# Performance work log

Hardware: AMD Instinct MI355X
Metric: run time of the kernel (lower is better)

The kernel has to match this reference:

```python
import jax, jax.numpy as jnp
import numpy as np

N_NODES = 20000   # atoms
N_EDGES = 320000  # bonds = line-graph nodes
N_ANGLES = 640000 # line-graph edges
N_GRAPHS = 256
NF = 92           # node_features
EF = 40           # edge_features (= RBF/ABF bins)
FC = 256
LAYERS = 3


def _bn(x, g, b):
    # BatchNorm1d in training mode: batch stats, biased variance, eps=1e-5
    mu = jnp.mean(x, axis=0)
    var = jnp.var(x, axis=0)
    return g * (x - mu) * jax.lax.rsqrt(var + 1e-5) + b


def _rbf(x, vmin, vmax, bins):
    centers = jnp.linspace(vmin, vmax, bins)
    gamma = 1.0 / (centers[1] - centers[0])  # 1/lengthscale (ALIGNN RBFExpansion)
    return jnp.exp(-gamma * (x[:, None] - centers) ** 2)


def _conv(src, dst, n_nodes, nf, ef, Ws, bs, Wd, bd, We, be, gm, bm, gn, bn2):
    # CGCNN conv: gather(u_add_v) + edge linear + BN + gated act + scatter-sum + BN + softplus residual
    h_src = nf @ Ws + bs                       # [N, 2F]
    h_dst = nf @ Wd + bd                       # [N, 2F]
    m = h_src[src] + h_dst[dst] + ef @ We + be # [E, 2F]
    m = _bn(m, gm, bm)
    h_f, h_s = jnp.split(m, 2, axis=1)
    m = jax.nn.sigmoid(h_f) * jax.nn.softplus(h_s)          # [E, F]
    h = jax.ops.segment_sum(m, dst, num_segments=n_nodes)   # scatter-sum to dst nodes
    h = _bn(h, gn, bn2)
    return jax.nn.softplus(nf + h)


def setup_inputs() -> dict:
    key = jax.random.key(0)
    ks = iter(jax.random.split(key, 64))
    rn = lambda *s: jax.random.normal(next(ks), s, dtype=jnp.float32)
    d = {}
    d['atom_features'] = rn(N_NODES, NF)
    d['r'] = rn(N_EDGES, 3) * 2.0  # bond vectors; norms land within RBF range [0, 8]
    d['angle_h'] = ((jax.random.uniform(next(ks), (N_ANGLES,), dtype=jnp.float32) - 0.5) * np.pi)
    d['g_src'] = jax.random.randint(next(ks), (N_EDGES,), 0, N_NODES, dtype=jnp.int32)
    d['g_dst'] = jax.random.randint(next(ks), (N_EDGES,), 0, N_NODES, dtype=jnp.int32)
    d['lg_src'] = jax.random.randint(next(ks), (N_ANGLES,), 0, N_EDGES, dtype=jnp.int32)
    d['lg_dst'] = jax.random.randint(next(ks), (N_ANGLES,), 0, N_EDGES, dtype=jnp.int32)
    d['node_gid'] = jnp.sort(jax.random.randint(next(ks), (N_NODES,), 0, N_GRAPHS, dtype=jnp.int32))
    d['emb_W'] = rn(NF, NF) * 0.1
    d['emb_b'] = jnp.zeros((NF,), jnp.float32)
    # conv layers on atom graph: node dim NF, edge dim EF, out 2*NF
    d['c1_Wsrc'] = rn(LAYERS, NF, 2 * NF) * 0.1
    d['c1_bsrc'] = jnp.zeros((LAYERS, 2 * NF), jnp.float32)
    d['c1_Wdst'] = rn(LAYERS, NF, 2 * NF) * 0.1
    d['c1_bdst'] = jnp.zeros((LAYERS, 2 * NF), jnp.float32)
    d['c1_Wedge'] = rn(LAYERS, EF, 2 * NF) * 0.1
    d['c1_bedge'] = jnp.zeros((LAYERS, 2 * NF), jnp.float32)
    d['c1_bnm_g'] = jnp.ones((LAYERS, 2 * NF), jnp.float32)
    d['c1_bnm_b'] = jnp.zeros((LAYERS, 2 * NF), jnp.float32)
    d['c1_bn_g'] = jnp.ones((LAYERS, NF), jnp.float32)
    d['c1_bn_b'] = jnp.zeros((LAYERS, NF), jnp.float32)
    # conv layers on line graph: node dim EF, edge dim EF, out 2*EF
    d['c2_Wsrc'] = rn(LAYERS, EF, 2 * EF) * 0.1
    d['c2_bsrc'] = jnp.zeros((LAYERS, 2 * EF), jnp.float32)
    d['c2_Wdst'] = rn(LAYERS, EF, 2 * EF) * 0.1
    d['c2_bdst'] = jnp.zeros((LAYERS, 2 * EF), jnp.float32)
    d['c2_Wedge'] = rn(LAYERS, EF, 2 * EF) * 0.1
    d['c2_bedge'] = jnp.zeros((LAYERS, 2 * EF), jnp.float32)
    d['c2_bnm_g'] = jnp.ones((LAYERS, 2 * EF), jnp.float32)
    d['c2_bnm_b'] = jnp.zeros((LAYERS, 2 * EF), jnp.float32)
    d['c2_bn_g'] = jnp.ones((LAYERS, EF), jnp.float32)
    d['c2_bn_b'] = jnp.zeros((LAYERS, EF), jnp.float32)
    d['fc_W'] = rn(NF, FC) * 0.1
    d['fc_b'] = jnp.zeros((FC,), jnp.float32)
    d['out_W'] = rn(FC, 1) * 0.1
    d['out_b'] = jnp.zeros((1,), jnp.float32)
    return d


def reference(atom_features, r, angle_h, g_src, g_dst, lg_src, lg_dst, node_gid,
              emb_W, emb_b,
              c1_Wsrc, c1_bsrc, c1_Wdst, c1_bdst, c1_Wedge, c1_bedge,
              c1_bnm_g, c1_bnm_b, c1_bn_g, c1_bn_b,
              c2_Wsrc, c2_bsrc, c2_Wdst, c2_bdst, c2_Wedge, c2_bedge,
              c2_bnm_g, c2_bnm_b, c2_bn_g, c2_bn_b,
              fc_W, fc_b, out_W, out_b):
    angle_features = _rbf(angle_h, -np.pi / 2, np.pi / 2, EF)      # [E2, EF]
    bondlength = jnp.linalg.norm(r, axis=1)                        # [E]
    edge_features = _rbf(bondlength, 0.0, 8.0, EF)                 # [E, EF]
    node_features = atom_features @ emb_W + emb_b                  # [N, NF]
    for i in range(LAYERS):
        node_features = _conv(g_src, g_dst, N_NODES, node_features, edge_features,
                              c1_Wsrc[i], c1_bsrc[i], c1_Wdst[i], c1_bdst[i],
                              c1_Wedge[i], c1_bedge[i], c1_bnm_g[i], c1_bnm_b[i],
                              c1_bn_g[i], c1_bn_b[i])
        edge_features = _conv(lg_src, lg_dst, N_EDGES, edge_features, angle_features,
                              c2_Wsrc[i], c2_bsrc[i], c2_Wdst[i], c2_bdst[i],
                              c2_Wedge[i], c2_bedge[i], c2_bnm_g[i], c2_bnm_b[i],
                              c2_bn_g[i], c2_bn_b[i])
    # AvgPooling readout over nodes per graph
    sums = jax.ops.segment_sum(node_features, node_gid, num_segments=N_GRAPHS)
    cnts = jax.ops.segment_sum(jnp.ones((N_NODES,), node_features.dtype), node_gid, num_segments=N_GRAPHS)
    feats = sums / jnp.maximum(cnts, 1.0)[:, None]                 # [G, NF]
    feats = jax.nn.softplus(feats)
    feats = jax.nn.softplus(feats @ fc_W + fc_b)                   # fc = Linear + Softplus, then extra softplus
    feats = jax.nn.softplus(feats)
    out = feats @ out_W + out_b                                    # [G, 1], link = identity
    return jnp.squeeze(out, axis=-1)                               # [G]
```

## Files before the change

### kernel.cpp

```cpp
#include <hip/hip_runtime.h>
#include <math.h>

#define N_NODES   20000
#define N_EDGESC  320000
#define N_ANGLESC 640000
#define N_GRAPHSC 256
#define NFDIM     92
#define EFDIM     40
#define FCDIM     256

typedef unsigned short u16;
typedef unsigned int u32;
typedef __attribute__((ext_vector_type(8))) short bf16x8;
typedef __attribute__((ext_vector_type(4))) float f32x4;

__device__ __forceinline__ u16 f2bf(float x) {
  union { float f; unsigned u; } v; v.f = x;
  unsigned r = v.u + 0x7fff + ((v.u >> 16) & 1);
  return (u16)(r >> 16);
}
__device__ __forceinline__ float bf2f(u16 h) {
  union { unsigned u; float f; } v; v.u = ((unsigned)h) << 16; return v.f;
}
__device__ __forceinline__ u32 pk2(float a, float b) {
  return (u32)f2bf(a) | ((u32)f2bf(b) << 16);
}
__device__ __forceinline__ float fsp(float x) {
  float e = __expf(-fabsf(x));
  return fmaxf(x, 0.f) + __logf(1.f + e);
}
__device__ __forceinline__ float fsig(float x) {
  float e = __expf(-x);
  return __builtin_amdgcn_rcpf(1.f + e);
}

__global__ void k_hist(const int* __restrict__ dst, int E, int* __restrict__ hist) {
  int e = blockIdx.x * blockDim.x + threadIdx.x;
  if (e < E) atomicAdd(&hist[dst[e]], 1);
}

__global__ void k_scan_pass1(const int* __restrict__ hist, int n, int* __restrict__ bsum) {
  __shared__ int buf[256];
  int i = blockIdx.x * 256 + threadIdx.x;
  buf[threadIdx.x] = (i < n) ? hist[i] : 0;
  __syncthreads();
  for (int o = 128; o > 0; o >>= 1) {
    if (threadIdx.x < o) buf[threadIdx.x] += buf[threadIdx.x + o];
    __syncthreads();
  }
  if (threadIdx.x == 0) bsum[blockIdx.x] = buf[0];
}

__global__ void k_scan_partials(int* __restrict__ bsum, int B) {
  __shared__ int buf[256];
  __shared__ int carry;
  if (threadIdx.x == 0) carry = 0;
  __syncthreads();
  for (int base = 0; base < B; base += 256) {
    int i = base + threadIdx.x;
    int v = (i < B) ? bsum[i] : 0;
    buf[threadIdx.x] = v;
    __syncthreads();
    for (int o = 1; o < 256; o <<= 1) {
      int t = (threadIdx.x >= o) ? buf[threadIdx.x - o] : 0;
      __syncthreads();
      buf[threadIdx.x] += t;
      __syncthreads();
    }
    if (i < B) bsum[i] = buf[threadIdx.x] - v + carry;
    int tile_total = buf[255];
    __syncthreads();
    if (threadIdx.x == 0) carry += tile_total;
    __syncthreads();
  }
}

__global__ void k_scan_pass3(const int* __restrict__ hist, int n, int total,
                             const int* __restrict__ bsum,
                             int* __restrict__ offsets, int* __restrict__ cursor) {
  __shared__ int buf[256];
  int i = blockIdx.x * 256 + threadIdx.x;
  int v = (i < n) ? hist[i] : 0;
  buf[threadIdx.x] = v;
  __syncthreads();
  for (int o = 1; o < 256; o <<= 1) {
    int t = (threadIdx.x >= o) ? buf[threadIdx.x - o] : 0;
    __syncthreads();
    buf[threadIdx.x] += t;
    __syncthreads();
  }
  int excl = buf[threadIdx.x] - v + bsum[blockIdx.x];
  if (i < n) {
    offsets[i] = excl;
    cursor[i] = excl;
    if (i == n - 1) offsets[n] = total;
  }
}

__global__ void k_fill(const int* __restrict__ dst, int E,
                       int* __restrict__ cursor, int* __restrict__ perm) {
  int e = blockIdx.x * blockDim.x + threadIdx.x;
  if (e >= E) return;
  int pos = atomicAdd(&cursor[dst[e]], 1);
  perm[pos] = e;
}

__global__ void k_sortbins(const int* __restrict__ offsets, int* __restrict__ perm, int nb) {
  int n = blockIdx.x * blockDim.x + threadIdx.x;
  if (n >= nb) return;
  int lo = offsets[n], hi = offsets[n + 1];
  for (int i = lo + 1; i < hi; i++) {
    int key = perm[i];
    int j = i - 1;
    while (j >= lo && perm[j] > key) { perm[j + 1] = perm[j]; j--; }
    perm[j + 1] = key;
  }
}

__global__ void k_invperm(const int* __restrict__ perm, int E, int* __restrict__ iperm) {
  int p = blockIdx.x * blockDim.x + threadIdx.x;
  if (p < E) iperm[perm[p]] = p;
}

__global__ void k_rbf_edge(const float* __restrict__ r, u16* __restrict__ ef) {
  int e = blockIdx.x * blockDim.x + threadIdx.x;
  if (e >= N_EDGESC) return;
  float x = r[e * 3 + 0], y = r[e * 3 + 1], z = r[e * 3 + 2];
  float bl = sqrtf(x * x + y * y + z * z);
  const float step = 8.f / 39.f;
  const float g = 39.f / 8.f;
  u32* o = (u32*)(ef + (long long)e * EFDIM);
#pragma unroll
  for (int i = 0; i < 20; i++) {
    float d0 = bl - (2 * i + 0) * step;
    float d1 = bl - (2 * i + 1) * step;
    o[i] = pk2(__expf(-g * d0 * d0), __expf(-g * d1 * d1));
  }
}

__global__ void k_gemm_bias(const float* __restrict__ A, const float* __restrict__ W,
                            const float* __restrict__ b, float* __restrict__ C,
                            int M, int N, int K) {
  int idx = blockIdx.x * blockDim.x + threadIdx.x;
  int total = M * N;
  if (idx >= total) return;
  int row = idx / N, col = idx - row * N;
  const float* a = A + (long long)row * K;
  float acc = b[col];
#pragma unroll 4
  for (int k = 0; k < K; k++) acc += a[k] * W[k * N + col];
  C[idx] = acc;
}

__global__ __launch_bounds__(256) void k_nf_gemm_b(
    const float* __restrict__ A, const float* __restrict__ W,
    const float* __restrict__ bias, u16* __restrict__ OUT) {
  __shared__ float As[64][93];
  __shared__ float Wls[92][64];
  __shared__ float bls[64];
  int t = threadIdx.x;
  int row0 = blockIdx.x * 64;
  int ct = blockIdx.y * 64;
  int cvalid = 184 - ct; if (cvalid > 64) cvalid = 64;
  for (int idx = t; idx < 64 * 92; idx += 256) {
    int rr = idx / 92, k = idx - rr * 92;
    int rg = row0 + rr;
    As[rr][k] = (rg < N_NODES) ? A[(long long)rg * 92 + k] : 0.f;
  }
  for (int idx = t; idx < 92 * 64; idx += 256) {
    int k = idx >> 6, c = idx & 63;
    Wls[k][c] = (c < cvalid) ? W[k * 184 + ct + c] : 0.f;
  }
  if (t < 64) bls[t] = (t < cvalid) ? bias[ct + t] : 0.f;
  __syncthreads();
  int rg = t >> 4, cg = t & 15;
  int r0 = rg * 4, c0 = cg * 4;
  float acc[4][4] = {};
#pragma unroll 2
  for (int k = 0; k < 92; k++) {
    float a0 = As[r0][k], a1 = As[r0 + 1][k], a2 = As[r0 + 2][k], a3 = As[r0 + 3][k];
    float4 w = *(float4*)&Wls[k][c0];
    acc[0][0] += a0 * w.x; acc[0][1] += a0 * w.y; acc[0][2] += a0 * w.z; acc[0][3] += a0 * w.w;
    acc[1][0] += a1 * w.x; acc[1][1] += a1 * w.y; acc[1][2] += a1 * w.z; acc[1][3] += a1 * w.w;
    acc[2][0] += a2 * w.x; acc[2][1] += a2 * w.y; acc[2][2] += a2 * w.z; acc[2][3] += a2 * w.w;
    acc[3][0] += a3 * w.x; acc[3][1] += a3 * w.y; acc[3][2] += a3 * w.z; acc[3][3] += a3 * w.w;
  }
  if (c0 < cvalid) {
    float b0 = bls[c0], b1 = bls[c0 + 1], b2 = bls[c0 + 2], b3 = bls[c0 + 3];
#pragma unroll
    for (int i = 0; i < 4; i++) {
      int rg2 = row0 + r0 + i;
      if (rg2 < N_NODES) {
        uint2 pkd;
        pkd.x = pk2(acc[i][0] + b0, acc[i][1] + b1);
        pkd.y = pk2(acc[i][2] + b2, acc[i][3] + b3);
        *(uint2*)(OUT + (long long)rg2 * 184 + ct + c0) = pkd;
      }
    }
  }
}

__global__ void k_mkwt1(const float* __restrict__ We, const float* __restrict__ be,
                        u16* __restrict__ WT1) {
  int idx = blockIdx.x * blockDim.x + threadIdx.x;
  if (idx >= 192 * 64) return;
  int c = idx >> 6, k = idx & 63;
  float v = 0.f;
  if (c < 184) {
    if (k < 40) v = We[k * 184 + c];
    else if (k == 40) v = be[c];
  }
  int b = 2 * k;
  int off = c * 128 + (((b >> 4) ^ (c & 7)) << 4) + (b & 15);
  WT1[off >> 1] = f2bf(v);
}

__global__ void k_mkwt2(const float* __restrict__ Ws, const float* __restrict__ bs,
                        const float* __restrict__ Wd, const float* __restrict__ bd,
                        const float* __restrict__ We, const float* __restrict__ be,
                        u16* __restrict__ WT2) {
  int idx = blockIdx.x * blockDim.x + threadIdx.x;
  if (idx >= 80 * 128) return;
  int c = idx >> 7, k = idx & 127;
  float v = 0.f;
  if (k < 40) v = Ws[k * 80 + c];
  else if (k < 80) v = Wd[(k - 40) * 80 + c];
  else if (k < 120) v = We[(k - 80) * 80 + c];
  else if (k == 120) v = bs[c] + bd[c] + be[c];
  int b = 2 * k;
  int off = c * 256 + (((b >> 4) ^ (c & 7)) << 4) + (b & 15);
  WT2[off >> 1] = f2bf(v);
}

__global__ __launch_bounds__(256) void k_conv1_mfma(
    const u16* __restrict__ EF, const int* __restrict__ src, const int* __restrict__ dst,
    const u16* __restrict__ HSb, const u16* __restrict__ HDb,
    const u16* __restrict__ WT1, const int* __restrict__ IPERM,
    u16* __restrict__ M, float* __restrict__ PART) {
  __shared__ __align__(16) char sA[64 * 128];
  __shared__ __align__(16) char sB[192 * 128];
  __shared__ float ssum[2][192];
  __shared__ int srcs[64], dsts[64], ipm[64];
  int t = threadIdx.x;
  int e0 = blockIdx.x * 64;
  for (int i = t; i < 2 * 192; i += 256) ((float*)ssum)[i] = 0.f;
  if (t < 64) {
    srcs[t] = src[e0 + t];
    dsts[t] = dst[e0 + t];
    ipm[t] = IPERM[e0 + t];
    uint4 z5 = {0x00003F80u, 0u, 0u, 0u};
    uint4 z = {0u, 0u, 0u, 0u};
    *(uint4*)(sA + t * 128 + ((5 ^ (t & 7)) << 4)) = z5;
    *(uint4*)(sA + t * 128 + ((6 ^ (t & 7)) << 4)) = z;
    *(uint4*)(sA + t * 128 + ((7 ^ (t & 7)) << 4)) = z;
  }
  {
    const uint4* efg = (const uint4*)EF;
    for (int i = t; i < 320; i += 256) {
      int r = i / 5, ch = i % 5;
      uint4 v = efg[(long long)(e0 + r) * 5 + ch];
      *(uint4*)(sA + r * 128 + ((ch ^ (r & 7)) << 4)) = v;
    }
  }
  {
    const uint4* wg = (const uint4*)WT1;
    uint4* bb = (uint4*)sB;
    for (int i = t; i < 1536; i += 256) bb[i] = wg[i];
  }
  __syncthreads();

  int lane = t & 63, w = t >> 6;
  int lr = lane & 15, lg = lane >> 4;
  int arow = w * 16 + lr;
  f32x4 zero = {0.f, 0.f, 0.f, 0.f};
  f32x4 acc[12];
#pragma unroll
  for (int n = 0; n < 12; n++) acc[n] = zero;
#pragma unroll
  for (int kt = 0; kt < 2; kt++) {
    bf16x8 a = *(const bf16x8*)(sA + arow * 128 + (((kt * 4 + lg) ^ (arow & 7)) << 4));
#pragma unroll
    for (int n = 0; n < 12; n++) {
      int brow = n * 16 + lr;
      bf16x8 b = *(const bf16x8*)(sB + brow * 128 + (((kt * 4 + lg) ^ (brow & 7)) << 4));
      acc[n] = __builtin_amdgcn_mfma_f32_16x16x32_bf16(a, b, acc[n], 0, 0, 0);
    }
  }
  __syncthreads();
  u16* stage = (u16*)sB;
  int base_r = w * 16 + lg * 4;
#pragma unroll
  for (int n = 0; n < 12; n++) {
    int col = n * 16 + lr;
    bool valid = col < 184;
    int pos = (col < 92) ? (2 * col) : (2 * (col - 92) + 1);
    float s = 0.f, q = 0.f;
#pragma unroll
    for (int j = 0; j < 4; j++) {
      int rr = base_r + j;
      float v = acc[n][j];
      if (valid) {
        v += bf2f(HSb[(long long)srcs[rr] * 184 + col]) + bf2f(HDb[(long long)dsts[rr] * 184 + col]);
        stage[rr * 192 + pos] = f2bf(v);
        s += v; q += v * v;
      }
    }
    s += __shfl_xor(s, 16, 64); s += __shfl_xor(s, 32, 64);
    q += __shfl_xor(q, 16, 64); q += __shfl_xor(q, 32, 64);
    if (valid && lg == 0) {
      atomicAdd(&ssum[0][col], s);
      atomicAdd(&ssum[1][col], q);
    }
  }
  __syncthreads();
  for (int i = t; i < 64 * 23; i += 256) {
    int rr = i / 23, ch = i - rr * 23;
    *(uint4*)(M + (long long)ipm[rr] * 184 + ch * 8) = *(const uint4*)(stage + rr * 192 + ch * 8);
  }
  float* P = PART + (long long)blockIdx.x * 368;
  for (int i = t; i < 184; i += 256) { P[i] = ssum[0][i]; P[184 + i] = ssum[1][i]; }
}

__global__ __launch_bounds__(256) void k_conv2_mfma(
    const u16* __restrict__ EF, const float* __restrict__ angle_h,
    const int* __restrict__ lsrc, const int* __restrict__ ldst,
    const u16* __restrict__ WT2, const int* __restrict__ IPERM,
    u16* __restrict__ M, float* __restrict__ PART) {
  __shared__ __align__(16) char sA[64 * 256];
  __shared__ __align__(16) char sB[80 * 256];
  __shared__ float ssum[2][80];
  __shared__ int srcl[64], dstl[64], ipm[64];
  __shared__ float hh[64];
  int t = threadIdx.x;
  int a0 = blockIdx.x * 64;
  if (t < 64) {
    srcl[t] = lsrc[a0 + t]; dstl[t] = ldst[a0 + t];
    hh[t] = angle_h[a0 + t]; ipm[t] = IPERM[a0 + t];
  }
  for (int i = t; i < 160; i += 256) ((float*)ssum)[i] = 0.f;
  __syncthreads();
  int lane = t & 63, w = t >> 6;
  if (w == 0) {
    int r = lane;
    const uint4* g = (const uint4*)EF + (long long)srcl[r] * 5;
#pragma unroll
    for (int ch = 0; ch < 5; ch++)
      *(uint4*)(sA + r * 256 + ((ch ^ (r & 7)) << 4)) = g[ch];
  } else if (w == 1) {
    int r = lane;
    const uint4* g = (const uint4*)EF + (long long)dstl[r] * 5;
#pragma unroll
    for (int ch = 0; ch < 5; ch++)
      *(uint4*)(sA + r * 256 + (((ch + 5) ^ (r & 7)) << 4)) = g[ch];
  } else {
    int r = lane;
    const float PI = 3.14159265358979323846f;
    const float step = PI / 39.f;
    const float gam = 39.f / PI;
    float h = hh[r];
    int k0 = (w == 2) ? 0 : 20;
#pragma unroll
    for (int p = 0; p < 10; p++) {
      int k = k0 + 2 * p;
      float d0 = h - (-PI * 0.5f + k * step);
      float d1 = h - (-PI * 0.5f + (k + 1) * step);
      u32 val = pk2(__expf(-gam * d0 * d0), __expf(-gam * d1 * d1));
      int b = 160 + 2 * k;
      *(u32*)(sA + r * 256 + (((b >> 4) ^ (r & 7)) << 4) + (b & 15)) = val;
    }
    if (w == 3) {
      uint4 z15 = {0x00003F80u, 0u, 0u, 0u};
      *(uint4*)(sA + r * 256 + ((15 ^ (r & 7)) << 4)) = z15;
    }
  }
  {
    const uint4* wg = (const uint4*)WT2;
    uint4* bb = (uint4*)sB;
    for (int i = t; i < 1280; i += 256) bb[i] = wg[i];
  }
  __syncthreads();

  int lr = lane & 15, lg = lane >> 4;
  int arow = w * 16 + lr;
  f32x4 zero = {0.f, 0.f, 0.f, 0.f};
  f32x4 acc[5];
#pragma unroll
  for (int n = 0; n < 5; n++) acc[n] = zero;
#pragma unroll
  for (int kt = 0; kt < 4; kt++) {
    bf16x8 a = *(const bf16x8*)(sA + arow * 256 + (((kt * 4 + lg) ^ (arow & 7)) << 4));
#pragma unroll
    for (int n = 0; n < 5; n++) {
      int brow = n * 16 + lr;
      bf16x8 b = *(const bf16x8*)(sB + brow * 256 + (((kt * 4 + lg) ^ (brow & 7)) << 4));
      acc[n] = __builtin_amdgcn_mfma_f32_16x16x32_bf16(a, b, acc[n], 0, 0, 0);
    }
  }
  __syncthreads();
  u16* stage = (u16*)sB;
  int base_r = w * 16 + lg * 4;
#pragma unroll
  for (int n = 0; n < 5; n++) {
    int col = n * 16 + lr;
    int pos = (col < 40) ? (2 * col) : (2 * (col - 40) + 1);
    float s = 0.f, q = 0.f;
#pragma unroll
    for (int j = 0; j < 4; j++) {
      float v = acc[n][j];
      stage[(base_r + j) * 80 + pos] = f2bf(v);
      s += v; q += v * v;
    }
    s += __shfl_xor(s, 16, 64); s += __shfl_xor(s, 32, 64);
    q += __shfl_xor(q, 16, 64); q += __shfl_xor(q, 32, 64);
    if (lg == 0) {
      atomicAdd(&ssum[0][col], s);
      atomicAdd(&ssum[1][col], q);
    }
  }
  __syncthreads();
  for (int i = t; i < 64 * 10; i += 256) {
    int rr = i / 10, ch = i - rr * 10;
    *(uint4*)(M + (long long)ipm[rr] * 80 + ch * 8) = *(const uint4*)(stage + rr * 80 + ch * 8);
  }
  float* P = PART + (long long)blockIdx.x * 160;
  for (int i = t; i < 80; i += 256) { P[i] = ssum[0][i]; P[80 + i] = ssum[1][i]; }
}

__global__ __launch_bounds__(256) void k_reduce_part(
    const float* __restrict__ part, int nblk, int C2, float* __restrict__ stat) {
  int chunks = gridDim.x;
  int per = (nblk + chunks - 1) / chunks;
  int lo = blockIdx.x * per;
  int hi = lo + per; if (hi > nblk) hi = nblk;
  if (lo >= hi) return;
  for (int c = threadIdx.x; c < C2; c += blockDim.x) {
    float s = 0.f;
    for (int b = lo; b < hi; b++) s += part[(long long)b * C2 + c];
    atomicAdd(&stat[c], s);
  }
}

__global__ void k_finalize(float* __restrict__ stat, const float* __restrict__ g,
                           const float* __restrict__ b, float* __restrict__ scsh,
                           int C, float invR) {
  int c = threadIdx.x + blockIdx.x * blockDim.x;
  if (c >= C) return;
  float mu = stat[c] * invR;
  float var = stat[C + c] * invR - mu * mu;
  float is = rsqrtf(var + 1e-5f);
  float sc = g[c] * is;
  scsh[c] = sc;
  scsh[C + c] = b[c] - mu * sc;
  stat[c] = 0.f;
  stat[C + c] = 0.f;
}

__global__ __launch_bounds__(512) void k_gather1(
    const u16* __restrict__ m, const int* __restrict__ offsets,
    const float* __restrict__ scsh, float* __restrict__ hagg, float* __restrict__ part) {
  __shared__ float sacc[4][92];
  int t = threadIdx.x;
  int ln = t >> 7, c = t & 127;
  int n = blockIdx.x * 4 + ln;
  if (c < 92) {
    float sc_f = scsh[c],       sh_f = scsh[184 + c];
    float sc_s = scsh[92 + c],  sh_s = scsh[276 + c];
    int lo = offsets[n], hi = offsets[n + 1];
    float acc = 0.f;
    for (int p = lo; p < hi; ++p) {
      u32 pr = *(const u32*)(m + (long long)p * 184 + 2 * c);
      float mf = bf2f((u16)(pr & 0xffffu)) * sc_f + sh_f;
      float ms = bf2f((u16)(pr >> 16)) * sc_s + sh_s;
      acc += fsig(mf) * fsp(ms);
    }
    hagg[(long long)n * 92 + c] = acc;
    sacc[ln][c] = acc;
  }
  __syncthreads();
  if (t < 184) {
    int cc = (t < 92) ? t : t - 92;
    bool sq = t >= 92;
    float s = 0.f;
#pragma unroll
    for (int b = 0; b < 4; b++) { float v = sacc[b][cc]; s += sq ? v * v : v; }
    part[(long long)blockIdx.x * 184 + t] = s;
  }
}

__global__ __launch_bounds__(320) void k_gather2(
    const u16* __restrict__ m, const int* __restrict__ offsets,
    const float* __restrict__ scsh, u16* __restrict__ hagg, float* __restrict__ part) {
  __shared__ float sacc[8][40];
  int t = threadIdx.x;
  int le = t / 40, c = t - le * 40;
  int e = blockIdx.x * 8 + le;
  float sc_f = scsh[c],      sh_f = scsh[80 + c];
  float sc_s = scsh[40 + c], sh_s = scsh[120 + c];
  int lo = offsets[e], hi = offsets[e + 1];
  float acc = 0.f;
  for (int p = lo; p < hi; ++p) {
    u32 pr = *(const u32*)(m + (long long)p * 80 + 2 * c);
    float mf = bf2f((u16)(pr & 0xffffu)) * sc_f + sh_f;
    float ms = bf2f((u16)(pr >> 16)) * sc_s + sh_s;
    acc += fsig(mf) * fsp(ms);
  }
  hagg[(long long)e * 40 + c] = f2bf(acc);
  sacc[le][c] = acc;
  __syncthreads();
  if (t < 80) {
    int cc = (t < 40) ? t : t - 40;
    bool sq = t >= 40;
    float s = 0.f;
#pragma unroll
    for (int b = 0; b < 8; b++) { float v = sacc[b][cc]; s += sq ? v * v : v; }
    part[(long long)blockIdx.x * 80 + t] = s;
  }
}

__global__ void k_bn_residual(const float* __restrict__ xin, const float* __restrict__ hagg,
                              const float* __restrict__ scsh, float* __restrict__ out,
                              int total, int C) {
  int idx = blockIdx.x * blockDim.x + threadIdx.x;
  if (idx >= total) return;
  int c = idx % C;
  out[idx] = fsp(xin[idx] + hagg[idx] * scsh[c] + scsh[C + c]);
}

__global__ void k_bn_residual_bb(u16* __restrict__ ef, const u16* __restrict__ hagg,
                                 const float* __restrict__ scsh, int total, int C) {
  int idx = blockIdx.x * blockDim.x + threadIdx.x;
  if (idx >= total) return;
  int c = idx % C;
  float v = fsp(bf2f(ef[idx]) + bf2f(hagg[idx]) * scsh[c] + scsh[C + c]);
  ef[idx] = f2bf(v);
}

__global__ __launch_bounds__(256) void k_head(
    const float* __restrict__ nf, const int* __restrict__ gid,
    const float* __restrict__ fcW, const float* __restrict__ fcb,
    const float* __restrict__ outW, const float* __restrict__ outb,
    float* __restrict__ out) {
  __shared__ float feats[NFDIM];
  __shared__ float warpsum[4];
  int g = blockIdx.x, t = threadIdx.x;
  int lo = 0, hi = N_NODES;
  while (lo < hi) { int mid = (lo + hi) >> 1; if (gid[mid] < g) lo = mid + 1; else hi = mid; }
  int lo2 = lo, hi2 = N_NODES;
  while (lo2 < hi2) { int mid = (lo2 + hi2) >> 1; if (gid[mid] < g + 1) lo2 = mid + 1; else hi2 = mid; }
  if (t < NFDIM) {
    float s = 0.f;
    for (int n = lo; n < lo2; ++n) s += nf[(long long)n * NFDIM + t];
    float cgt = fmaxf((float)(lo2 - lo), 1.f);
    feats[t] = fsp(s / cgt);
  }
  __syncthreads();
  float acc = fcb[t];
#pragma unroll 4
  for (int k = 0; k < NFDIM; k++) acc += feats[k] * fcW[k * FCDIM + t];
  float z = fsp(fsp(acc));
  float v = z * outW[t];
  for (int off = 32; off > 0; off >>= 1) v += __shfl_down(v, off, 64);
  if ((t & 63) == 0) warpsum[t >> 6] = v;
  __syncthreads();
  if (t == 0) out[g] = warpsum[0] + warpsum[1] + warpsum[2] + warpsum[3] + outb[0];
}

__global__ void k_sentinel(float* out, float v) {
  int i = blockIdx.x * blockDim.x + threadIdx.x;
  if (i < N_GRAPHSC) out[i] = v;
}

static inline int cdiv(long long a, long long b) { return (int)((a + b - 1) / b); }

extern "C" void kernel_launch(void* const* d_in, const int* in_sizes, int n_in,
                              void* d_out, int out_size, void* d_ws, size_t ws_size,
                              hipStream_t stream) {
  (void)in_sizes; (void)n_in; (void)out_size;
  const float* atom_features = (const float*)d_in[0];
  const float* r             = (const float*)d_in[1];
  const float* angle_h       = (const float*)d_in[2];
  const int*   g_src         = (const int*)d_in[3];
  const int*   g_dst         = (const int*)d_in[4];
  const int*   lg_src        = (const int*)d_in[5];
  const int*   lg_dst        = (const int*)d_in[6];
  const int*   node_gid      = (const int*)d_in[7];
  const float* emb_W         = (const float*)d_in[8];
  const float* emb_b         = (const float*)d_in[9];
  const float* c1_Wsrc       = (const float*)d_in[10];
  const float* c1_bsrc       = (const float*)d_in[11];
  const float* c1_Wdst       = (const float*)d_in[12];
  const float* c1_bdst       = (const float*)d_in[13];
  const float* c1_Wedge      = (const float*)d_in[14];
  const float* c1_bedge      = (const float*)d_in[15];
  const float* c1_bnm_g      = (const float*)d_in[16];
  const float* c1_bnm_b      = (const float*)d_in[17];
  const float* c1_bn_g       = (const float*)d_in[18];
  const float* c1_bn_b       = (const float*)d_in[19];
  const float* c2_Wsrc       = (const float*)d_in[20];
  const float* c2_bsrc       = (const float*)d_in[21];
  const float* c2_Wdst       = (const float*)d_in[22];
  const float* c2_bdst       = (const float*)d_in[23];
  const float* c2_Wedge      = (const float*)d_in[24];
  const float* c2_bedge      = (const float*)d_in[25];
  const float* c2_bnm_g      = (const float*)d_in[26];
  const float* c2_bnm_b      = (const float*)d_in[27];
  const float* c2_bn_g       = (const float*)d_in[28];
  const float* c2_bn_b       = (const float*)d_in[29];
  const float* fc_W          = (const float*)d_in[30];
  const float* fc_b          = (const float*)d_in[31];
  const float* out_W         = (const float*)d_in[32];
  const float* out_b         = (const float*)d_in[33];

  char* basep = (char*)d_ws;
  size_t off = 0;
  auto walloc = [&](size_t bytes) {
    char* p = basep + off;
    off += (bytes + 255) & ~(size_t)255;
    return p;
  };
  u16*   M     = (u16*)walloc((size_t)58880000 * 2);
  u16*   EF    = (u16*)walloc((size_t)12800000 * 2);
  float* NF    = (float*)walloc((size_t)1840000 * 4);
  u16*   HS1   = (u16*)walloc((size_t)3680000 * 2);
  u16*   HD1   = (u16*)walloc((size_t)3680000 * 2);
  float* HAGG1 = (float*)walloc((size_t)1840000 * 4);
  u16*   HAGG2 = (u16*)walloc((size_t)12800000 * 2);
  float* PART  = (float*)walloc((size_t)3200000 * 4);
  int*   HIST  = (int*)walloc((size_t)320000 * 4);
  int*   OFF1  = (int*)walloc((size_t)20001 * 4);
  int*   CUR1  = (int*)walloc((size_t)20000 * 4);
  int*   PERM1 = (int*)walloc((size_t)320000 * 4);
  int*   IPERM1= (int*)walloc((size_t)320000 * 4);
  int*   OFF2  = (int*)walloc((size_t)320001 * 4);
  int*   CUR2  = (int*)walloc((size_t)320000 * 4);
  int*   PERM2 = (int*)walloc((size_t)640000 * 4);
  int*   IPERM2= (int*)walloc((size_t)640000 * 4);
  int*   BSUM  = (int*)walloc((size_t)2048 * 4);
  u16*   WT1   = (u16*)walloc((size_t)192 * 64 * 2);
  u16*   WT2   = (u16*)walloc((size_t)80 * 128 * 2);
  float* STAT  = (float*)walloc(512 * 4);
  float* SCSHM = (float*)walloc(1024 * 4);
  float* SCSHN = (float*)walloc(512 * 4);
  if (ws_size < off) {
    k_sentinel<<<1, 256, 0, stream>>>((float*)d_out, (float)(ws_size >> 20));
    return;
  }

  hipMemsetAsync(STAT, 0, 512 * sizeof(float), stream);

  {
    int NB = N_NODES, E = N_EDGESC;
    int B = cdiv(NB, 256);
    hipMemsetAsync(HIST, 0, (size_t)NB * 4, stream);
    k_hist<<<cdiv(E, 256), 256, 0, stream>>>(g_dst, E, HIST);
    k_scan_pass1<<<B, 256, 0, stream>>>(HIST, NB, BSUM);
    k_scan_partials<<<1, 256, 0, stream>>>(BSUM, B);
    k_scan_pass3<<<B, 256, 0, stream>>>(HIST, NB, E, BSUM, OFF1, CUR1);
    k_fill<<<cdiv(E, 256), 256, 0, stream>>>(g_dst, E, CUR1, PERM1);
    k_sortbins<<<cdiv(NB, 256), 256, 0, stream>>>(OFF1, PERM1, NB);
    k_invperm<<<cdiv(E, 256), 256, 0, stream>>>(PERM1, E, IPERM1);
  }
  {
    int NB = N_EDGESC, E = N_ANGLESC;
    int B = cdiv(NB, 256);
    hipMemsetAsync(HIST, 0, (size_t)NB * 4, stream);
    k_hist<<<cdiv(E, 256), 256, 0, stream>>>(lg_dst, E, HIST);
    k_scan_pass1<<<B, 256, 0, stream>>>(HIST, NB, BSUM);
    k_scan_partials<<<1, 256, 0, stream>>>(BSUM, B);
    k_scan_pass3<<<B, 256, 0, stream>>>(HIST, NB, E, BSUM, OFF2, CUR2);
    k_fill<<<cdiv(E, 256), 256, 0, stream>>>(lg_dst, E, CUR2, PERM2);
    k_sortbins<<<cdiv(NB, 256), 256, 0, stream>>>(OFF2, PERM2, NB);
    k_invperm<<<cdiv(E, 256), 256, 0, stream>>>(PERM2, E, IPERM2);
  }

  k_rbf_edge<<<cdiv(N_EDGESC, 256), 256, 0, stream>>>(r, EF);
  k_gemm_bias<<<cdiv((long long)N_NODES * NFDIM, 256), 256, 0, stream>>>(
      atom_features, emb_W, emb_b, NF, N_NODES, NFDIM, NFDIM);

  dim3 gNF(cdiv(N_NODES, 64), 3);

  for (int i = 0; i < 3; i++) {
    k_mkwt1<<<48, 256, 0, stream>>>(c1_Wedge + i * EFDIM * 2 * NFDIM, c1_bedge + i * 2 * NFDIM, WT1);
    k_nf_gemm_b<<<gNF, 256, 0, stream>>>(NF, c1_Wsrc + i * NFDIM * 2 * NFDIM, c1_bsrc + i * 2 * NFDIM, HS1);
    k_nf_gemm_b<<<gNF, 256, 0, stream>>>(NF, c1_Wdst + i * NFDIM * 2 * NFDIM, c1_bdst + i * 2 * NFDIM, HD1);
    k_conv1_mfma<<<N_EDGESC / 64, 256, 0, stream>>>(EF, g_src, g_dst, HS1, HD1, WT1, IPERM1, M, PART);
    k_reduce_part<<<256, 256, 0, stream>>>(PART, N_EDGESC / 64, 368, STAT);
    k_finalize<<<1, 256, 0, stream>>>(STAT, c1_bnm_g + i * 184, c1_bnm_b + i * 184, SCSHM, 184, 1.f / N_EDGESC);
    k_gather1<<<N_NODES / 4, 512, 0, stream>>>(M, OFF1, SCSHM, HAGG1, PART);
    k_reduce_part<<<256, 256, 0, stream>>>(PART, N_NODES / 4, 184, STAT);
    k_finalize<<<1, 256, 0, stream>>>(STAT, c1_bn_g + i * 92, c1_bn_b + i * 92, SCSHN, 92, 1.f / N_NODES);
    k_bn_residual<<<cdiv((long long)N_NODES * NFDIM, 256), 256, 0, stream>>>(
        NF, HAGG1, SCSHN, NF, N_NODES * NFDIM, NFDIM);

    k_mkwt2<<<40, 256, 0, stream>>>(
        c2_Wsrc + i * EFDIM * 2 * EFDIM, c2_bsrc + i * 2 * EFDIM,
        c2_Wdst + i * EFDIM * 2 * EFDIM, c2_bdst + i * 2 * EFDIM,
        c2_Wedge + i * EFDIM * 2 * EFDIM, c2_bedge + i * 2 * EFDIM, WT2);
    k_conv2_mfma<<<N_ANGLESC / 64, 256, 0, stream>>>(EF, angle_h, lg_src, lg_dst, WT2, IPERM2, M, PART);
    k_reduce_part<<<256, 256, 0, stream>>>(PART, N_ANGLESC / 64, 160, STAT);
    k_finalize<<<1, 256, 0, stream>>>(STAT, c2_bnm_g + i * 80, c2_bnm_b + i * 80, SCSHM, 80, 1.f / N_ANGLESC);
    k_gather2<<<N_EDGESC / 8, 320, 0, stream>>>(M, OFF2, SCSHM, HAGG2, PART);
    k_reduce_part<<<256, 256, 0, stream>>>(PART, N_EDGESC / 8, 80, STAT);
    k_finalize<<<1, 256, 0, stream>>>(STAT, c2_bn_g + i * 40, c2_bn_b + i * 40, SCSHN, 40, 1.f / N_EDGESC);
    k_bn_residual_bb<<<cdiv((long long)N_EDGESC * EFDIM, 256), 256, 0, stream>>>(
        EF, HAGG2, SCSHN, N_EDGESC * EFDIM, EFDIM);
  }

  k_head<<<N_GRAPHSC, 256, 0, stream>>>(NF, node_gid, fc_W, fc_b, out_W, out_b, (float*)d_out);
}
```

Before: 1.768 ms.

## Fuse node src/dst projections into conv1 MFMA via gathered bf16 node features

Replaces the two per-layer node GEMMs (HS/HD) and their per-edge gathers with a single K=256 MFMA in the conv1 kernel. Each edge row concatenates bf16 source-node features, destination-node features, edge features and a bias column, and is multiplied by a stacked weight matrix. This removes two kernel launches and the scattered 2-byte HS/HD reads, in exchange for about 4x more MFMA work per edge, a weight tile streamed through LDS in 8 synchronized chunks, and a new bf16 conversion kernel for node features. Node features are now rounded to bf16 before the projection, which changes numerical precision.

After: 1.622 ms. 1.09x faster.

```diff
diff --git a/kernel.cpp b/kernel.cpp
--- a/kernel.cpp
+++ b/kernel.cpp
@@ -152,67 +152,32 @@
   C[idx] = acc;
 }
 
-__global__ __launch_bounds__(256) void k_nf_gemm_b(
-    const float* __restrict__ A, const float* __restrict__ W,
-    const float* __restrict__ bias, u16* __restrict__ OUT) {
-  __shared__ float As[64][93];
-  __shared__ float Wls[92][64];
-  __shared__ float bls[64];
-  int t = threadIdx.x;
-  int row0 = blockIdx.x * 64;
-  int ct = blockIdx.y * 64;
-  int cvalid = 184 - ct; if (cvalid > 64) cvalid = 64;
-  for (int idx = t; idx < 64 * 92; idx += 256) {
-    int rr = idx / 92, k = idx - rr * 92;
-    int rg = row0 + rr;
-    As[rr][k] = (rg < N_NODES) ? A[(long long)rg * 92 + k] : 0.f;
-  }
-  for (int idx = t; idx < 92 * 64; idx += 256) {
-    int k = idx >> 6, c = idx & 63;
-    Wls[k][c] = (c < cvalid) ? W[k * 184 + ct + c] : 0.f;
-  }
-  if (t < 64) bls[t] = (t < cvalid) ? bias[ct + t] : 0.f;
-  __syncthreads();
-  int rg = t >> 4, cg = t & 15;
-  int r0 = rg * 4, c0 = cg * 4;
-  float acc[4][4] = {};
-#pragma unroll 2
-  for (int k = 0; k < 92; k++) {
-    float a0 = As[r0][k], a1 = As[r0 + 1][k], a2 = As[r0 + 2][k], a3 = As[r0 + 3][k];
-    float4 w = *(float4*)&Wls[k][c0];
-    acc[0][0] += a0 * w.x; acc[0][1] += a0 * w.y; acc[0][2] += a0 * w.z; acc[0][3] += a0 * w.w;
-    acc[1][0] += a1 * w.x; acc[1][1] += a1 * w.y; acc[1][2] += a1 * w.z; acc[1][3] += a1 * w.w;
-    acc[2][0] += a2 * w.x; acc[2][1] += a2 * w.y; acc[2][2] += a2 * w.z; acc[2][3] += a2 * w.w;
-    acc[3][0] += a3 * w.x; acc[3][1] += a3 * w.y; acc[3][2] += a3 * w.z; acc[3][3] += a3 * w.w;
-  }
-  if (c0 < cvalid) {
-    float b0 = bls[c0], b1 = bls[c0 + 1], b2 = bls[c0 + 2], b3 = bls[c0 + 3];
-#pragma unroll
-    for (int i = 0; i < 4; i++) {
-      int rg2 = row0 + r0 + i;
-      if (rg2 < N_NODES) {
-        uint2 pkd;
-        pkd.x = pk2(acc[i][0] + b0, acc[i][1] + b1);
-        pkd.y = pk2(acc[i][2] + b2, acc[i][3] + b3);
-        *(uint2*)(OUT + (long long)rg2 * 184 + ct + c0) = pkd;
-      }
-    }
-  }
-}
-
-__global__ void k_mkwt1(const float* __restrict__ We, const float* __restrict__ be,
-                        u16* __restrict__ WT1) {
+__global__ void k_nf2b(const float* __restrict__ NF, u16* __restrict__ NFb) {
   int idx = blockIdx.x * blockDim.x + threadIdx.x;
-  if (idx >= 192 * 64) return;
-  int c = idx >> 6, k = idx & 63;
+  if (idx >= N_NODES * 96) return;
+  int n = idx / 96, c = idx - n * 96;
+  NFb[idx] = (c < 92) ? f2bf(NF[(long long)n * 92 + c]) : (u16)0;
+}
+
+__global__ void k_mkwt1f(const float* __restrict__ Wsrc, const float* __restrict__ bsrc,
+                         const float* __restrict__ Wdst, const float* __restrict__ bdst,
+                         const float* __restrict__ We, const float* __restrict__ be,
+                         u16* __restrict__ WT1F) {
+  int idx = blockIdx.x * blockDim.x + threadIdx.x;
+  if (idx >= 32 * 192 * 8) return;
+  int j = idx & 7;
+  int qc = idx >> 3;
+  int c = qc % 192;
+  int q = qc / 192;
+  int k = q * 8 + j;
   float v = 0.f;
   if (c < 184) {
-    if (k < 40) v = We[k * 184 + c];
-    else if (k == 40) v = be[c];
-  }
-  int b = 2 * k;
-  int off = c * 128 + (((b >> 4) ^ (c & 7)) << 4) + (b & 15);
-  WT1[off >> 1] = f2bf(v);
+    if (k < 92) v = Wsrc[k * 184 + c];
+    else if (k >= 96 && k < 188) v = Wdst[(k - 96) * 184 + c];
+    else if (k >= 192 && k < 232) v = We[(k - 192) * 184 + c];
+    else if (k == 232) v = bsrc[c] + bdst[c] + be[c];
+  }
+  WT1F[idx] = f2bf(v);
 }
 
 __global__ void k_mkwt2(const float* __restrict__ Ws, const float* __restrict__ bs,
@@ -232,13 +197,13 @@
   WT2[off >> 1] = f2bf(v);
 }
 
-__global__ __launch_bounds__(256) void k_conv1_mfma(
-    const u16* __restrict__ EF, const int* __restrict__ src, const int* __restrict__ dst,
-    const u16* __restrict__ HSb, const u16* __restrict__ HDb,
-    const u16* __restrict__ WT1, const int* __restrict__ IPERM,
+__global__ __launch_bounds__(256) void k_conv1_mfma2(
+    const u16* __restrict__ NFb, const u16* __restrict__ EF,
+    const int* __restrict__ src, const int* __restrict__ dst,
+    const u16* __restrict__ WT1F, const int* __restrict__ IPERM,
     u16* __restrict__ M, float* __restrict__ PART) {
-  __shared__ __align__(16) char sA[64 * 128];
-  __shared__ __align__(16) char sB[192 * 128];
+  __shared__ __align__(16) char sA[64 * 512];
+  __shared__ __align__(16) char sBc[4 * 192 * 16];
   __shared__ float ssum[2][192];
   __shared__ int srcs[64], dsts[64], ipm[64];
   int t = threadIdx.x;
@@ -248,74 +213,86 @@
     srcs[t] = src[e0 + t];
     dsts[t] = dst[e0 + t];
     ipm[t] = IPERM[e0 + t];
-    uint4 z5 = {0x00003F80u, 0u, 0u, 0u};
-    uint4 z = {0u, 0u, 0u, 0u};
-    *(uint4*)(sA + t * 128 + ((5 ^ (t & 7)) << 4)) = z5;
-    *(uint4*)(sA + t * 128 + ((6 ^ (t & 7)) << 4)) = z;
-    *(uint4*)(sA + t * 128 + ((7 ^ (t & 7)) << 4)) = z;
-  }
+  }
+  __syncthreads();
+  int lane = t & 63, w = t >> 6;
   {
-    const uint4* efg = (const uint4*)EF;
-    for (int i = t; i < 320; i += 256) {
-      int r = i / 5, ch = i % 5;
-      uint4 v = efg[(long long)(e0 + r) * 5 + ch];
-      *(uint4*)(sA + r * 128 + ((ch ^ (r & 7)) << 4)) = v;
-    }
-  }
-  {
-    const uint4* wg = (const uint4*)WT1;
-    uint4* bb = (uint4*)sB;
-    for (int i = t; i < 1536; i += 256) bb[i] = wg[i];
-  }
-  __syncthreads();
-
-  int lane = t & 63, w = t >> 6;
+    int r = lane;
+    if (w == 0) {
+      const uint4* g = (const uint4*)(NFb + (long long)srcs[r] * 96);
+#pragma unroll
+      for (int ch = 0; ch < 12; ch++)
+        *(uint4*)(sA + r * 512 + ((ch ^ (r & 7)) << 4)) = g[ch];
+    } else if (w == 1) {
+      const uint4* g = (const uint4*)(NFb + (long long)dsts[r] * 96);
+#pragma unroll
+      for (int ch = 0; ch < 12; ch++)
+        *(uint4*)(sA + r * 512 + (((ch + 12) ^ (r & 7)) << 4)) = g[ch];
+    } else if (w == 2) {
+      const uint4* g = (const uint4*)(EF + (long long)(e0 + r) * 40);
+#pragma unroll
+      for (int ch = 0; ch < 5; ch++)
+        *(uint4*)(sA + r * 512 + (((ch + 24) ^ (r & 7)) << 4)) = g[ch];
+    } else {
+      uint4 zb = {0x00003F80u, 0u, 0u, 0u};
+      uint4 z = {0u, 0u, 0u, 0u};
+      *(uint4*)(sA + r * 512 + ((29 ^ (r & 7)) << 4)) = zb;
+      *(uint4*)(sA + r * 512 + ((30 ^ (r & 7)) << 4)) = z;
+      *(uint4*)(sA + r * 512 + ((31 ^ (r & 7)) << 4)) = z;
+    }
+  }
   int lr = lane & 15, lg = lane >> 4;
   int arow = w * 16 + lr;
   f32x4 zero = {0.f, 0.f, 0.f, 0.f};
   f32x4 acc[12];
 #pragma unroll
   for (int n = 0; n < 12; n++) acc[n] = zero;
-#pragma unroll
-  for (int kt = 0; kt < 2; kt++) {
-    bf16x8 a = *(const bf16x8*)(sA + arow * 128 + (((kt * 4 + lg) ^ (arow & 7)) << 4));
+  const uint4* wsrc4 = (const uint4*)WT1F;
+  for (int kt = 0; kt < 8; kt++) {
+    __syncthreads();
+    {
+      uint4* bb = (uint4*)sBc;
+      int base = kt * 768;
+#pragma unroll
+      for (int i = 0; i < 3; i++) bb[t + i * 256] = wsrc4[base + t + i * 256];
+    }
+    __syncthreads();
+    int q = kt * 4 + lg;
+    bf16x8 a = *(const bf16x8*)(sA + arow * 512 + ((q ^ (arow & 7)) << 4));
 #pragma unroll
     for (int n = 0; n < 12; n++) {
-      int brow = n * 16 + lr;
-      bf16x8 b = *(const bf16x8*)(sB + brow * 128 + (((kt * 4 + lg) ^ (brow & 7)) << 4));
+      bf16x8 b = *(const bf16x8*)(sBc + ((lg * 192 + n * 16 + lr) << 4));
       acc[n] = __builtin_amdgcn_mfma_f32_16x16x32_bf16(a, b, acc[n], 0, 0, 0);
     }
   }
   __syncthreads();
-  u16* stage = (u16*)sB;
+  u16* stage = (u16*)sA;
   int base_r = w * 16 + lg * 4;
 #pragma unroll
   for (int n = 0; n < 12; n++) {
     int col = n * 16 + lr;
     bool valid = col < 184;
     int pos = (col < 92) ? (2 * col) : (2 * (col - 92) + 1);
-    float s = 0.f, q = 0.f;
+    float s = 0.f, q2 = 0.f;
 #pragma unroll
     for (int j = 0; j < 4; j++) {
-      int rr = base_r + j;
       float v = acc[n][j];
       if (valid) {
-        v += bf2f(HSb[(long long)srcs[rr] * 184 + col]) + bf2f(HDb[(long long)dsts[rr] * 184 + col]);
-        stage[rr * 192 + pos] = f2bf(v);
-        s += v; q += v * v;
+        stage[(base_r + j) * 196 + pos] = f2bf(v);
+        s += v; q2 += v * v;
       }
     }
     s += __shfl_xor(s, 16, 64); s += __shfl_xor(s, 32, 64);
-    q += __shfl_xor(q, 16, 64); q += __shfl_xor(q, 32, 64);
+    q2 += __shfl_xor(q2, 16, 64); q2 += __shfl_xor(q2, 32, 64);
     if (valid && lg == 0) {
       atomicAdd(&ssum[0][col], s);
-      atomicAdd(&ssum[1][col], q);
-    }
-  }
-  __syncthreads();
-  for (int i = t; i < 64 * 23; i += 256) {
-    int rr = i / 23, ch = i - rr * 23;
-    *(uint4*)(M + (long long)ipm[rr] * 184 + ch * 8) = *(const uint4*)(stage + rr * 192 + ch * 8);
+      atomicAdd(&ssum[1][col], q2);
+    }
+  }
+  __syncthreads();
+  for (int i = t; i < 64 * 46; i += 256) {
+    int rr = i / 46, ch = i - rr * 46;
+    *(uint2*)(M + (long long)ipm[rr] * 184 + ch * 4) = *(const uint2*)(stage + rr * 196 + ch * 4);
   }
   float* P = PART + (long long)blockIdx.x * 368;
   for (int i = t; i < 184; i += 256) { P[i] = ssum[0][i]; P[184 + i] = ssum[1][i]; }
@@ -621,8 +598,7 @@
   u16*   M     = (u16*)walloc((size_t)58880000 * 2);
   u16*   EF    = (u16*)walloc((size_t)12800000 * 2);
   float* NF    = (float*)walloc((size_t)1840000 * 4);
-  u16*   HS1   = (u16*)walloc((size_t)3680000 * 2);
-  u16*   HD1   = (u16*)walloc((size_t)3680000 * 2);
+  u16*   NFb   = (u16*)walloc((size_t)20000 * 96 * 2);
   float* HAGG1 = (float*)walloc((size_t)1840000 * 4);
   u16*   HAGG2 = (u16*)walloc((size_t)12800000 * 2);
   float* PART  = (float*)walloc((size_t)3200000 * 4);
@@ -636,7 +612,7 @@
   int*   PERM2 = (int*)walloc((size_t)640000 * 4);
   int*   IPERM2= (int*)walloc((size_t)640000 * 4);
   int*   BSUM  = (int*)walloc((size_t)2048 * 4);
-  u16*   WT1   = (u16*)walloc((size_t)192 * 64 * 2);
+  u16*   WT1F  = (u16*)walloc((size_t)32 * 192 * 8 * 2);
   u16*   WT2   = (u16*)walloc((size_t)80 * 128 * 2);
   float* STAT  = (float*)walloc(512 * 4);
   float* SCSHM = (float*)walloc(1024 * 4);
@@ -676,14 +652,14 @@
   k_rbf_edge<<<cdiv(N_EDGESC, 256), 256, 0, stream>>>(r, EF);
   k_gemm_bias<<<cdiv((long long)N_NODES * NFDIM, 256), 256, 0, stream>>>(
       atom_features, emb_W, emb_b, NF, N_NODES, NFDIM, NFDIM);
-
-  dim3 gNF(cdiv(N_NODES, 64), 3);
+  k_nf2b<<<cdiv((long long)N_NODES * 96, 256), 256, 0, stream>>>(NF, NFb);
 
   for (int i = 0; i < 3; i++) {
-    k_mkwt1<<<48, 256, 0, stream>>>(c1_Wedge + i * EFDIM * 2 * NFDIM, c1_bedge + i * 2 * NFDIM, WT1);
-    k_nf_gemm_b<<<gNF, 256, 0, stream>>>(NF, c1_Wsrc + i * NFDIM * 2 * NFDIM, c1_bsrc + i * 2 * NFDIM, HS1);
-    k_nf_gemm_b<<<gNF, 256, 0, stream>>>(NF, c1_Wdst + i * NFDIM * 2 * NFDIM, c1_bdst + i * 2 * NFDIM, HD1);
-    k_conv1_mfma<<<N_EDGESC / 64, 256, 0, stream>>>(EF, g_src, g_dst, HS1, HD1, WT1, IPERM1, M, PART);
+    k_mkwt1f<<<cdiv(32 * 192 * 8, 256), 256, 0, stream>>>(
+        c1_Wsrc + i * NFDIM * 2 * NFDIM, c1_bsrc + i * 2 * NFDIM,
+        c1_Wdst + i * NFDIM * 2 * NFDIM, c1_bdst + i * 2 * NFDIM,
+        c1_Wedge + i * EFDIM * 2 * NFDIM, c1_bedge + i * 2 * NFDIM, WT1F);
+    k_conv1_mfma2<<<N_EDGESC / 64, 256, 0, stream>>>(NFb, EF, g_src, g_dst, WT1F, IPERM1, M, PART);
     k_reduce_part<<<256, 256, 0, stream>>>(PART, N_EDGESC / 64, 368, STAT);
     k_finalize<<<1, 256, 0, stream>>>(STAT, c1_bnm_g + i * 184, c1_bnm_b + i * 184, SCSHM, 184, 1.f / N_EDGESC);
     k_gather1<<<N_NODES / 4, 512, 0, stream>>>(M, OFF1, SCSHM, HAGG1, PART);
@@ -691,6 +667,7 @@
     k_finalize<<<1, 256, 0, stream>>>(STAT, c1_bn_g + i * 92, c1_bn_b + i * 92, SCSHN, 92, 1.f / N_NODES);
     k_bn_residual<<<cdiv((long long)N_NODES * NFDIM, 256), 256, 0, stream>>>(
         NF, HAGG1, SCSHN, NF, N_NODES * NFDIM, NFDIM);
+    k_nf2b<<<cdiv((long long)N_NODES * 96, 256), 256, 0, stream>>>(NF, NFb);
 
     k_mkwt2<<<40, 256, 0, stream>>>(
         c2_Wsrc + i * EFDIM * 2 * EFDIM, c2_bsrc + i * 2 * EFDIM,
```
